# Performance work log

Measured on AMD Instinct MI355X. Metric: run time of the kernel, lower is better.

## Reference

```python
import jax, jax.numpy as jnp
import numpy as np

N_NODES, N_EDGES = 100000, 1600000
D_IN, D_HID, D_OUT = 128, 128, 64


def setup_inputs() -> dict:
    key = jax.random.key(0)
    k = jax.random.split(key, 6)
    x = jax.random.normal(k[0], (N_NODES, D_IN), dtype=jnp.float32)
    edge_index = jax.random.randint(k[1], (2, N_EDGES), 0, N_NODES, dtype=jnp.int32)
    # GCNConv params: W stored as [in, out] for right-multiply, glorot-ish scale
    W1 = jax.random.normal(k[2], (D_IN, D_HID), dtype=jnp.float32) * (1.0 / np.sqrt(D_IN))
    b1 = jnp.zeros((D_HID,), dtype=jnp.float32)
    W2 = jax.random.normal(k[3], (D_HID, D_OUT), dtype=jnp.float32) * (1.0 / np.sqrt(D_HID))
    b2 = jnp.zeros((D_OUT,), dtype=jnp.float32)
    return {"x": x, "edge_index": edge_index, "W1": W1, "b1": b1, "W2": W2, "b2": b2}


def reference(x, edge_index, W1, b1, W2, b2):
    N = x.shape[0]
    loops = jnp.arange(N, dtype=edge_index.dtype)
    src = jnp.concatenate([edge_index[0], loops])  # [E+N]
    dst = jnp.concatenate([edge_index[1], loops])  # [E+N]
    # symmetric GCN normalization (deg over targets, incl. self loops)
    deg = jax.ops.segment_sum(jnp.ones_like(dst, dtype=x.dtype), dst, num_segments=N)
    dinv = jnp.where(deg > 0, jax.lax.rsqrt(deg), 0.0)
    norm = dinv[src] * dinv[dst]  # [E+N]

    def gcn(h, W, b):
        h = h @ W                         # [N, out]
        msg = h[src] * norm[:, None]      # gather + scale, [E+N, out]
        return jax.ops.segment_sum(msg, dst, num_segments=N) + b

    h = jax.nn.relu(gcn(x, W1, b1))  # Dropout is identity in eval
    return gcn(h, W2, b2)
```

## Files before the change

kernel.cpp:

```cpp
#include <hip/hip_runtime.h>


#define D_IN  128
#define D_HID 128
#define D_OUT 64
#define NBSHIFT 9
#define SEG 10240

typedef short short8 __attribute__((ext_vector_type(8)));
typedef float floatx4 __attribute__((ext_vector_type(4)));

__device__ __forceinline__ unsigned short f2bf(float f) {
    unsigned int u = __float_as_uint(f);
    u += 0x7fffu + ((u >> 16) & 1u);
    return (unsigned short)(u >> 16);
}
__device__ __forceinline__ float bf2f(unsigned short h) {
    return __uint_as_float((unsigned int)h << 16);
}
__device__ __forceinline__ float bf_lo(unsigned int u) { return __uint_as_float(u << 16); }
__device__ __forceinline__ float bf_hi(unsigned int u) { return __uint_as_float(u & 0xffff0000u); }


__device__ __forceinline__ void wsplit_one(const float* __restrict__ W,
                                           unsigned short* __restrict__ Ws,
                                           int id, int DOUT_, int HALF) {
    int i = id & 7;
    int lane = (id >> 3) & 63;
    int ctkt = id >> 9;
    int NCT = DOUT_ / 16;
    int ct = ctkt % NCT, kt = ctkt / NCT;
    int k = kt * 32 + ((lane >> 4) << 3) + i;
    int n = ct * 16 + (lane & 15);
    float v = W[(size_t)k * DOUT_ + n];
    unsigned short h = f2bf(v);
    Ws[id] = h;
    Ws[HALF + id] = f2bf(v - bf2f(h));
}

__global__ __launch_bounds__(256) void k_prep(const float* __restrict__ W1,
                                              const float* __restrict__ W2,
                                              unsigned short* __restrict__ w1s,
                                              unsigned short* __restrict__ w2s,
                                              unsigned short* __restrict__ h1b,
                                              unsigned short* __restrict__ h2b,
                                              int* __restrict__ bcur, int N) {
    int id = blockIdx.x * 256 + threadIdx.x;
    if (id < 16384) wsplit_one(W1, w1s, id, D_HID, 16384);
    if (id < 8192)  wsplit_one(W2, w2s, id, D_OUT, 8192);
    if (id < 128)   h1b[(size_t)N * 128 + id] = 0;
    if (id < 64)    h2b[(size_t)N * 64 + id] = 0;
    if (id < 256)   bcur[id] = 0;
}


__global__ __launch_bounds__(256) void k_bin(const int* __restrict__ src,
                                             const int* __restrict__ dst,
                                             int* __restrict__ ebuf,
                                             int* __restrict__ bcur, int E, int NB) {
    __shared__ int h[256];
    __shared__ int basep[256];
    const int t = threadIdx.x;
    h[t] = 0;
    __syncthreads();
    const int base = blockIdx.x * 4096;
    int s[16], d[16];
#pragma unroll
    for (int k = 0; k < 16; ++k) {
        int e = base + k * 256 + t;
        bool v = e < E;
        s[k] = v ? src[e] : 0;
        d[k] = v ? dst[e] : -1;
        if (v) atomicAdd(&h[d[k] >> NBSHIFT], 1);
    }
    __syncthreads();
    if (t < NB && h[t]) basep[t] = atomicAdd(&bcur[t], h[t]);
    __syncthreads();
    h[t] = 0;
    __syncthreads();
#pragma unroll
    for (int k = 0; k < 16; ++k) {
        if (d[k] >= 0) {
            int b = d[k] >> NBSHIFT;
            int r = atomicAdd(&h[b], 1);
            ebuf[(size_t)b * SEG + basep[b] + r] = (s[k] << 9) | (d[k] & 511);
        }
    }
}

__global__ __launch_bounds__(256) void k_bfill(const int* __restrict__ ebuf,
                                               const int* __restrict__ bcur,
                                               int* __restrict__ csr,
                                               int* __restrict__ nodeinfo,
                                               float* __restrict__ dinv,
                                               int N) {
    __shared__ int cnt[512];
    __shared__ int pref[512];
    __shared__ int tsum[256];
    const int t = threadIdx.x;
    const int b = blockIdx.x;
    const int nb0 = b << NBSHIFT;
    const int NN = min(512, N - nb0);
    const int ec = bcur[b];
    const int* __restrict__ eb = ebuf + (size_t)b * SEG;

    cnt[t] = 0;
    cnt[t + 256] = 0;
    __syncthreads();
    for (int e = t; e < ec; e += 256) atomicAdd(&cnt[eb[e] & 511], 1);
    __syncthreads();

    int a0 = cnt[2 * t], a1 = cnt[2 * t + 1];
    tsum[t] = a0 + a1;
    __syncthreads();
    for (int off = 1; off < 256; off <<= 1) {
        int y = (t >= off) ? tsum[t - off] : 0;
        __syncthreads();
        tsum[t] += y;
        __syncthreads();
    }
    int excl = tsum[t] - (a0 + a1);
    pref[2 * t] = excl;
    pref[2 * t + 1] = excl + a0;
    __syncthreads();

    const int segbase = b * SEG;
    for (int nl = t; nl < NN; nl += 256) {
        int deg = cnt[nl];
        nodeinfo[nb0 + nl] = ((segbase + pref[nl]) << 10) | deg;
        dinv[nb0 + nl] = rsqrtf((float)(deg + 1));
    }
    __syncthreads();

    for (int e = t; e < ec; e += 256) {
        int v = eb[e];
        int r = atomicAdd(&pref[v & 511], 1);
        csr[segbase + r] = (unsigned)v >> 9;
    }
}


template <int DOUT_>
__global__ __launch_bounds__(256) void mfma_gemm(const float* __restrict__ X,
                                                 const unsigned short* __restrict__ Wsplit,
                                                 const float* __restrict__ dinv,
                                                 unsigned short* __restrict__ Hb,
                                                 int N) {
    constexpr int NCT = DOUT_ / 16;
    constexpr int HALF = 4 * NCT * 64 * 8;
    __shared__ unsigned short lds[2 * HALF];

    const int t = threadIdx.x;
    {
        const int4* s4 = (const int4*)Wsplit;
        int4* d4 = (int4*)lds;
        constexpr int NV = 2 * HALF / 8;
        for (int i = t; i < NV; i += 256) d4[i] = s4[i];
    }
    __syncthreads();

    const int wave = t >> 6, lane = t & 63;
    const int grow = blockIdx.x * 64 + wave * 16 + (lane & 15);
    const int rowc = min(grow, N - 1);
    const int kl = (lane >> 4) << 3;

    floatx4 acc[NCT];
#pragma unroll
    for (int c = 0; c < NCT; ++c) acc[c] = (floatx4)0.f;

#pragma unroll
    for (int kt = 0; kt < 4; ++kt) {
        const float* xp = X + (size_t)rowc * 128 + kt * 32 + kl;
        float4 a0 = *(const float4*)xp;
        float4 a1 = *(const float4*)(xp + 4);
        float xs[8] = {a0.x, a0.y, a0.z, a0.w, a1.x, a1.y, a1.z, a1.w};
        short8 ah, al;
#pragma unroll
        for (int i = 0; i < 8; ++i) {
            unsigned short h = f2bf(xs[i]);
            ah[i] = (short)h;
            al[i] = (short)f2bf(xs[i] - bf2f(h));
        }
#pragma unroll
        for (int c = 0; c < NCT; ++c) {
            const int off = ((kt * NCT + c) * 64 + lane) * 8;
            short8 bh = *(const short8*)&lds[off];
            short8 bl = *(const short8*)&lds[HALF + off];
            acc[c] = __builtin_amdgcn_mfma_f32_16x16x32_bf16(ah, bh, acc[c], 0, 0, 0);
            acc[c] = __builtin_amdgcn_mfma_f32_16x16x32_bf16(al, bh, acc[c], 0, 0, 0);
            acc[c] = __builtin_amdgcn_mfma_f32_16x16x32_bf16(ah, bl, acc[c], 0, 0, 0);
        }
    }

    const int orow = blockIdx.x * 64 + wave * 16 + ((lane >> 4) << 2);
#pragma unroll
    for (int r = 0; r < 4; ++r) {
        int gr = orow + r;
        if (gr < N) {
            float dn = dinv[gr];
#pragma unroll
            for (int c = 0; c < NCT; ++c)
                Hb[(size_t)gr * DOUT_ + c * 16 + (lane & 15)] = f2bf(acc[c][r] * dn);
        }
    }
}


template <int DOUT_>
__global__ __launch_bounds__(256) void mfma_gemm_b(const unsigned short* __restrict__ Xb,
                                                   const unsigned short* __restrict__ Wsplit,
                                                   const float* __restrict__ dinv,
                                                   unsigned short* __restrict__ Hb,
                                                   int N) {
    constexpr int NCT = DOUT_ / 16;
    constexpr int HALF = 4 * NCT * 64 * 8;
    __shared__ unsigned short lds[2 * HALF];

    const int t = threadIdx.x;
    {
        const int4* s4 = (const int4*)Wsplit;
        int4* d4 = (int4*)lds;
        constexpr int NV = 2 * HALF / 8;
        for (int i = t; i < NV; i += 256) d4[i] = s4[i];
    }
    __syncthreads();

    const int wave = t >> 6, lane = t & 63;
    const int grow = blockIdx.x * 64 + wave * 16 + (lane & 15);
    const int rowc = min(grow, N - 1);
    const int kl = (lane >> 4) << 3;

    floatx4 acc[NCT];
#pragma unroll
    for (int c = 0; c < NCT; ++c) acc[c] = (floatx4)0.f;

#pragma unroll
    for (int kt = 0; kt < 4; ++kt) {
        short8 ah = *(const short8*)(Xb + (size_t)rowc * 128 + kt * 32 + kl);
#pragma unroll
        for (int c = 0; c < NCT; ++c) {
            const int off = ((kt * NCT + c) * 64 + lane) * 8;
            short8 bh = *(const short8*)&lds[off];
            short8 bl = *(const short8*)&lds[HALF + off];
            acc[c] = __builtin_amdgcn_mfma_f32_16x16x32_bf16(ah, bh, acc[c], 0, 0, 0);
            acc[c] = __builtin_amdgcn_mfma_f32_16x16x32_bf16(ah, bl, acc[c], 0, 0, 0);
        }
    }

    const int orow = blockIdx.x * 64 + wave * 16 + ((lane >> 4) << 2);
#pragma unroll
    for (int r = 0; r < 4; ++r) {
        int gr = orow + r;
        if (gr < N) {
            float dn = dinv[gr];
#pragma unroll
            for (int c = 0; c < NCT; ++c)
                Hb[(size_t)gr * DOUT_ + c * 16 + (lane & 15)] = f2bf(acc[c][r] * dn);
        }
    }
}


__global__ __launch_bounds__(256) void agg1_kernel(const uint4* __restrict__ H4,
                                                   const int* __restrict__ nodeinfo,
                                                   const int* __restrict__ csr_src,
                                                   const float* __restrict__ dinv,
                                                   const float* __restrict__ bias,
                                                   unsigned short* __restrict__ outb,
                                                   int N, int NBK) {
    const int xcd = blockIdx.x & 7;
    const int ch  = xcd >> 2;
    const int nb  = (blockIdx.x >> 3) * 4 + (xcd & 3);
    if (nb >= NBK) return;
    const int t = threadIdx.x;
    const int wave = t >> 6, lane = t & 63;
    const int g = lane >> 3, gl = lane & 7;
    const int n = nb * 32 + wave * 8 + g;
    const bool live = n < N;
    const int v = live ? nodeinfo[n] : 0;
    const int e0 = (unsigned)v >> 10;
    const int deg = v & 1023;
    int m = deg;
    m = max(m, __shfl_xor(m, 8));
    m = max(m, __shfl_xor(m, 16));
    m = max(m, __shfl_xor(m, 32));

    const int cb = ch * 8;
    float acc[8] = {0.f, 0.f, 0.f, 0.f, 0.f, 0.f, 0.f, 0.f};
    for (int eb = 0; eb < m; eb += 8) {
        int s_l = (eb + gl < deg)
                      ? __builtin_nontemporal_load(csr_src + e0 + eb + gl)
                      : N;
        int sj[8]; uint4 u[8];
#pragma unroll
        for (int q = 0; q < 8; ++q) sj[q] = __shfl(s_l, (g << 3) | q);
#pragma unroll
        for (int q = 0; q < 8; ++q) u[q] = H4[(size_t)sj[q] * 16 + cb + gl];
#pragma unroll
        for (int q = 0; q < 8; ++q) {
            acc[0] += bf_lo(u[q].x); acc[1] += bf_hi(u[q].x);
            acc[2] += bf_lo(u[q].y); acc[3] += bf_hi(u[q].y);
            acc[4] += bf_lo(u[q].z); acc[5] += bf_hi(u[q].z);
            acc[6] += bf_lo(u[q].w); acc[7] += bf_hi(u[q].w);
        }
    }
    uint4 us = H4[(size_t)(live ? n : N) * 16 + cb + gl];
    acc[0] += bf_lo(us.x); acc[1] += bf_hi(us.x);
    acc[2] += bf_lo(us.y); acc[3] += bf_hi(us.y);
    acc[4] += bf_lo(us.z); acc[5] += bf_hi(us.z);
    acc[6] += bf_lo(us.w); acc[7] += bf_hi(us.w);

    if (live) {
        const float dn = dinv[n];
        const float* bp = bias + ch * 64 + gl * 8;
        unsigned short o[8];
#pragma unroll
        for (int j = 0; j < 8; ++j)
            o[j] = f2bf(fmaxf(fmaf(acc[j], dn, bp[j]), 0.f));
        *reinterpret_cast<int4*>(&outb[(size_t)n * 128 + ch * 64 + gl * 8]) =
            *reinterpret_cast<const int4*>(o);
    }
}

__global__ __launch_bounds__(256) void agg2_kernel(const uint2* __restrict__ H2,
                                                   const int* __restrict__ nodeinfo,
                                                   const int* __restrict__ csr_src,
                                                   const float* __restrict__ dinv,
                                                   const float* __restrict__ bias,
                                                   float* __restrict__ out,
                                                   int N, int NBK) {
    const int xcd = blockIdx.x & 7;
    const int ch  = xcd >> 2;
    const int nb  = (blockIdx.x >> 3) * 4 + (xcd & 3);
    if (nb >= NBK) return;
    const int t = threadIdx.x;
    const int wave = t >> 6, lane = t & 63;
    const int g = lane >> 3, gl = lane & 7;
    const int n = nb * 32 + wave * 8 + g;
    const bool live = n < N;
    const int v = live ? nodeinfo[n] : 0;
    const int e0 = (unsigned)v >> 10;
    const int deg = v & 1023;
    int m = deg;
    m = max(m, __shfl_xor(m, 8));
    m = max(m, __shfl_xor(m, 16));
    m = max(m, __shfl_xor(m, 32));

    const int cb = ch * 8;
    float acc[4] = {0.f, 0.f, 0.f, 0.f};
    for (int eb = 0; eb < m; eb += 8) {
        int s_l = (eb + gl < deg)
                      ? __builtin_nontemporal_load(csr_src + e0 + eb + gl)
                      : N;
        int sj[8]; uint2 u[8];
#pragma unroll
        for (int q = 0; q < 8; ++q) sj[q] = __shfl(s_l, (g << 3) | q);
#pragma unroll
        for (int q = 0; q < 8; ++q) u[q] = H2[(size_t)sj[q] * 16 + cb + gl];
#pragma unroll
        for (int q = 0; q < 8; ++q) {
            acc[0] += bf_lo(u[q].x); acc[1] += bf_hi(u[q].x);
            acc[2] += bf_lo(u[q].y); acc[3] += bf_hi(u[q].y);
        }
    }
    uint2 us = H2[(size_t)(live ? n : N) * 16 + cb + gl];
    acc[0] += bf_lo(us.x); acc[1] += bf_hi(us.x);
    acc[2] += bf_lo(us.y); acc[3] += bf_hi(us.y);

    if (live) {
        const float dn = dinv[n];
        const int c0 = ch * 32 + gl * 4;
        const float* bp = bias + c0;
        floatx4 o;
        o.x = fmaf(acc[0], dn, bp[0]);
        o.y = fmaf(acc[1], dn, bp[1]);
        o.z = fmaf(acc[2], dn, bp[2]);
        o.w = fmaf(acc[3], dn, bp[3]);
        __builtin_nontemporal_store(o, reinterpret_cast<floatx4*>(&out[(size_t)n * 64 + c0]));
    }
}


extern "C" void kernel_launch(void* const* d_in, const int* in_sizes, int n_in,
                              void* d_out, int out_size, void* d_ws, size_t ws_size,
                              hipStream_t stream) {
    const float* x  = (const float*)d_in[0];
    const int*   ei = (const int*)d_in[1];
    const float* W1 = (const float*)d_in[2];
    const float* b1 = (const float*)d_in[3];
    const float* W2 = (const float*)d_in[4];
    const float* b2 = (const float*)d_in[5];
    float* out = (float*)d_out;

    const int N = in_sizes[0] / D_IN;
    const int E = in_sizes[1] / 2;
    const int* src = ei;
    const int* dst = ei + E;
    const int NB = (N + 511) >> NBSHIFT;

    char* w = (char*)d_ws;
    auto alloc = [&](size_t bytes) {
        char* p = w;
        w += (bytes + 255) & ~(size_t)255;
        return p;
    };
    int*   nodeinfo  = (int*)alloc((size_t)N * 4);
    float* dinv      = (float*)alloc((size_t)N * 4);
    int*   csr       = (int*)alloc((size_t)NB * SEG * 4);
    unsigned short* h1b = (unsigned short*)alloc((size_t)(N + 1) * D_HID * 2);
    unsigned short* h2b = (unsigned short*)alloc((size_t)(N + 1) * D_OUT * 2);
    unsigned short* hgb = (unsigned short*)alloc((size_t)N * D_HID * 2);
    int*   bcur      = (int*)alloc(256 * 4);
    unsigned short* w1s = (unsigned short*)alloc(2 * 16384 * 2);
    unsigned short* w2s = (unsigned short*)alloc(2 * 8192 * 2);
    int*   ebuf      = (int*)hgb;

    k_prep<<<64, 256, 0, stream>>>(W1, W2, w1s, w2s, h1b, h2b, bcur, N);
    k_bin<<<(E + 4095) / 4096, 256, 0, stream>>>(src, dst, ebuf, bcur, E, NB);
    k_bfill<<<NB, 256, 0, stream>>>(ebuf, bcur, csr, nodeinfo, dinv, N);

    mfma_gemm<D_HID><<<(N + 63) / 64, 256, 0, stream>>>(x, w1s, dinv, h1b, N);

    const int NBK = (N + 31) / 32;
    agg1_kernel<<<((NBK + 3) / 4) * 8, 256, 0, stream>>>((const uint4*)h1b, nodeinfo, csr,
                                                         dinv, b1, hgb, N, NBK);
    mfma_gemm_b<D_OUT><<<(N + 63) / 64, 256, 0, stream>>>(hgb, w2s, dinv, h2b, N);
    agg2_kernel<<<((NBK + 3) / 4) * 8, 256, 0, stream>>>((const uint2*)h2b, nodeinfo, csr,
                                                         dinv, b2, out, N, NBK);
}
```

Measured before the change: 205.1 us.

## Halve GEMM LDS footprint, drop split-x MFMA term, use cached CSR loads

```diff
diff --git a/kernel.cpp b/kernel.cpp
--- a/kernel.cpp
+++ b/kernel.cpp
@@ -148,17 +148,10 @@
                                                  int N) {
     constexpr int NCT = DOUT_ / 16;
     constexpr int HALF = 4 * NCT * 64 * 8;
-    __shared__ unsigned short lds[2 * HALF];
-
-    const int t = threadIdx.x;
-    {
-        const int4* s4 = (const int4*)Wsplit;
-        int4* d4 = (int4*)lds;
-        constexpr int NV = 2 * HALF / 8;
-        for (int i = t; i < NV; i += 256) d4[i] = s4[i];
-    }
-    __syncthreads();
-
+    constexpr int LHALF = 2 * NCT * 64 * 8;
+    __shared__ unsigned short lds[2 * LHALF];
+
+    const int t = threadIdx.x;
     const int wave = t >> 6, lane = t & 63;
     const int grow = blockIdx.x * 64 + wave * 16 + (lane & 15);
     const int rowc = min(grow, N - 1);
@@ -169,26 +162,37 @@
     for (int c = 0; c < NCT; ++c) acc[c] = (floatx4)0.f;
 
 #pragma unroll
-    for (int kt = 0; kt < 4; ++kt) {
-        const float* xp = X + (size_t)rowc * 128 + kt * 32 + kl;
-        float4 a0 = *(const float4*)xp;
-        float4 a1 = *(const float4*)(xp + 4);
-        float xs[8] = {a0.x, a0.y, a0.z, a0.w, a1.x, a1.y, a1.z, a1.w};
-        short8 ah, al;
-#pragma unroll
-        for (int i = 0; i < 8; ++i) {
-            unsigned short h = f2bf(xs[i]);
-            ah[i] = (short)h;
-            al[i] = (short)f2bf(xs[i] - bf2f(h));
-        }
-#pragma unroll
-        for (int c = 0; c < NCT; ++c) {
-            const int off = ((kt * NCT + c) * 64 + lane) * 8;
-            short8 bh = *(const short8*)&lds[off];
-            short8 bl = *(const short8*)&lds[HALF + off];
-            acc[c] = __builtin_amdgcn_mfma_f32_16x16x32_bf16(ah, bh, acc[c], 0, 0, 0);
-            acc[c] = __builtin_amdgcn_mfma_f32_16x16x32_bf16(al, bh, acc[c], 0, 0, 0);
-            acc[c] = __builtin_amdgcn_mfma_f32_16x16x32_bf16(ah, bl, acc[c], 0, 0, 0);
+    for (int s = 0; s < 2; ++s) {
+        __syncthreads();
+        {
+            const int4* s4h = (const int4*)(Wsplit + s * LHALF);
+            const int4* s4l = (const int4*)(Wsplit + HALF + s * LHALF);
+            int4* d4 = (int4*)lds;
+            constexpr int NV = LHALF / 8;
+            for (int i = t; i < NV; i += 256) {
+                d4[i] = s4h[i];
+                d4[NV + i] = s4l[i];
+            }
+        }
+        __syncthreads();
+#pragma unroll
+        for (int ktl = 0; ktl < 2; ++ktl) {
+            const int kt = s * 2 + ktl;
+            const float* xp = X + (size_t)rowc * 128 + kt * 32 + kl;
+            float4 a0 = *(const float4*)xp;
+            float4 a1 = *(const float4*)(xp + 4);
+            float xs[8] = {a0.x, a0.y, a0.z, a0.w, a1.x, a1.y, a1.z, a1.w};
+            short8 ah;
+#pragma unroll
+            for (int i = 0; i < 8; ++i) ah[i] = (short)f2bf(xs[i]);
+#pragma unroll
+            for (int c = 0; c < NCT; ++c) {
+                const int off = ((ktl * NCT + c) * 64 + lane) * 8;
+                short8 bh = *(const short8*)&lds[off];
+                short8 bl = *(const short8*)&lds[LHALF + off];
+                acc[c] = __builtin_amdgcn_mfma_f32_16x16x32_bf16(ah, bh, acc[c], 0, 0, 0);
+                acc[c] = __builtin_amdgcn_mfma_f32_16x16x32_bf16(ah, bl, acc[c], 0, 0, 0);
+            }
         }
     }
 
@@ -214,17 +218,10 @@
                                                    int N) {
     constexpr int NCT = DOUT_ / 16;
     constexpr int HALF = 4 * NCT * 64 * 8;
-    __shared__ unsigned short lds[2 * HALF];
-
-    const int t = threadIdx.x;
-    {
-        const int4* s4 = (const int4*)Wsplit;
-        int4* d4 = (int4*)lds;
-        constexpr int NV = 2 * HALF / 8;
-        for (int i = t; i < NV; i += 256) d4[i] = s4[i];
-    }
-    __syncthreads();
-
+    constexpr int LHALF = 2 * NCT * 64 * 8;
+    __shared__ unsigned short lds[2 * LHALF];
+
+    const int t = threadIdx.x;
     const int wave = t >> 6, lane = t & 63;
     const int grow = blockIdx.x * 64 + wave * 16 + (lane & 15);
     const int rowc = min(grow, N - 1);
@@ -235,15 +232,31 @@
     for (int c = 0; c < NCT; ++c) acc[c] = (floatx4)0.f;
 
 #pragma unroll
-    for (int kt = 0; kt < 4; ++kt) {
-        short8 ah = *(const short8*)(Xb + (size_t)rowc * 128 + kt * 32 + kl);
-#pragma unroll
-        for (int c = 0; c < NCT; ++c) {
-            const int off = ((kt * NCT + c) * 64 + lane) * 8;
-            short8 bh = *(const short8*)&lds[off];
-            short8 bl = *(const short8*)&lds[HALF + off];
-            acc[c] = __builtin_amdgcn_mfma_f32_16x16x32_bf16(ah, bh, acc[c], 0, 0, 0);
-            acc[c] = __builtin_amdgcn_mfma_f32_16x16x32_bf16(ah, bl, acc[c], 0, 0, 0);
+    for (int s = 0; s < 2; ++s) {
+        __syncthreads();
+        {
+            const int4* s4h = (const int4*)(Wsplit + s * LHALF);
+            const int4* s4l = (const int4*)(Wsplit + HALF + s * LHALF);
+            int4* d4 = (int4*)lds;
+            constexpr int NV = LHALF / 8;
+            for (int i = t; i < NV; i += 256) {
+                d4[i] = s4h[i];
+                d4[NV + i] = s4l[i];
+            }
+        }
+        __syncthreads();
+#pragma unroll
+        for (int ktl = 0; ktl < 2; ++ktl) {
+            const int kt = s * 2 + ktl;
+            short8 ah = *(const short8*)(Xb + (size_t)rowc * 128 + kt * 32 + kl);
+#pragma unroll
+            for (int c = 0; c < NCT; ++c) {
+                const int off = ((ktl * NCT + c) * 64 + lane) * 8;
+                short8 bh = *(const short8*)&lds[off];
+                short8 bl = *(const short8*)&lds[LHALF + off];
+                acc[c] = __builtin_amdgcn_mfma_f32_16x16x32_bf16(ah, bh, acc[c], 0, 0, 0);
+                acc[c] = __builtin_amdgcn_mfma_f32_16x16x32_bf16(ah, bl, acc[c], 0, 0, 0);
+            }
         }
     }
 
@@ -288,9 +301,7 @@
     const int cb = ch * 8;
     float acc[8] = {0.f, 0.f, 0.f, 0.f, 0.f, 0.f, 0.f, 0.f};
     for (int eb = 0; eb < m; eb += 8) {
-        int s_l = (eb + gl < deg)
-                      ? __builtin_nontemporal_load(csr_src + e0 + eb + gl)
-                      : N;
+        int s_l = (eb + gl < deg) ? csr_src[e0 + eb + gl] : N;
         int sj[8]; uint4 u[8];
 #pragma unroll
         for (int q = 0; q < 8; ++q) sj[q] = __shfl(s_l, (g << 3) | q);
@@ -349,9 +360,7 @@
     const int cb = ch * 8;
     float acc[4] = {0.f, 0.f, 0.f, 0.f};
     for (int eb = 0; eb < m; eb += 8) {
-        int s_l = (eb + gl < deg)
-                      ? __builtin_nontemporal_load(csr_src + e0 + eb + gl)
-                      : N;
+        int s_l = (eb + gl < deg) ? csr_src[e0 + eb + gl] : N;
         int sj[8]; uint2 u[8];
 #pragma unroll
         for (int q = 0; q < 8; ++q) sj[q] = __shfl(s_l, (g << 3) | q);
```

Result: faster. 190.2 us (-7.3%).
